# Kernel optimization log

Hardware: AMD Instinct MI355X
Metric: run time of the kernel (lower is better)

Reference implementation:

```python
import jax, jax.numpy as jnp
from jax import lax
import numpy as np

SCALE, K_UP = 2, 5


def conv2d(x, w, pad=0, dil=1):
    return lax.conv_general_dilated(x, w, (1, 1), [(pad, pad), (pad, pad)],
                                    rhs_dilation=(dil, dil),
                                    dimension_numbers=('NCHW', 'OIHW', 'NCHW'))


def cbr(x, w, g, b, pad=0, relu=True):
    # Conv (no bias) + BatchNorm (eval: running_mean=0, running_var=1, eps=1e-5) + optional ReLU
    x = conv2d(x, w, pad)
    x = x * (g / jnp.sqrt(1.0 + 1e-5))[None, :, None, None] + b[None, :, None, None]
    return jnp.maximum(x, 0.0) if relu else x


def resize_bilinear_ac(x, ho, wo):
    # bilinear interpolation, align_corners=True (matches F.interpolate)
    B, C, H, W = x.shape
    ys = jnp.linspace(0.0, H - 1.0, ho)
    xs = jnp.linspace(0.0, W - 1.0, wo)
    y0 = jnp.floor(ys).astype(jnp.int32); y1 = jnp.minimum(y0 + 1, H - 1)
    x0 = jnp.floor(xs).astype(jnp.int32); x1 = jnp.minimum(x0 + 1, W - 1)
    wy = (ys - y0).astype(x.dtype)
    wx = (xs - x0).astype(x.dtype)
    top = x[:, :, y0, :]
    bot = x[:, :, y1, :]
    v = top * (1.0 - wy)[None, None, :, None] + bot * wy[None, None, :, None]
    return v[:, :, :, x0] * (1.0 - wx) + v[:, :, :, x1] * wx


def setup_inputs() -> dict:
    key = jax.random.key(0)
    ks = jax.random.split(key, 10)
    B, CH, CL, H, W = 4, 256, 128, 64, 64
    CMID, CO, IC, KENC = 64, 128, 64, 3

    def wgt(k, shape):
        fan = int(np.prod(shape[1:]))
        return (jax.random.normal(k, shape, jnp.float32) / np.sqrt(fan)).astype(jnp.float32)

    d = {}
    d['x_h'] = jax.random.normal(ks[0], (B, CH, H, W), jnp.float32)
    d['x_l'] = jax.random.normal(ks[1], (B, CL, H * SCALE, W * SCALE), jnp.float32)
    d['w_reduce'] = wgt(ks[2], (IC, CH, 3, 3)); d['g_reduce'] = jnp.ones(IC); d['b_reduce'] = jnp.zeros(IC)
    d['w1'] = wgt(ks[3], (CMID, CH, 1, 1)); d['g1'] = jnp.ones(CMID); d['b1'] = jnp.zeros(CMID)
    d['w2'] = wgt(ks[4], (CMID, CL, 1, 1)); d['g2'] = jnp.ones(CMID); d['b2'] = jnp.zeros(CMID)
    d['w_enc'] = wgt(ks[5], (K_UP * K_UP, 2 * CMID, KENC, KENC)); d['g_enc'] = jnp.ones(K_UP * K_UP); d['b_enc'] = jnp.zeros(K_UP * K_UP)
    d['w_out1'] = wgt(ks[6], (CO, IC + CL, 3, 3)); d['g_out1'] = jnp.ones(CO); d['b_out1'] = jnp.zeros(CO)
    d['w_out2'] = wgt(ks[7], (CO, CO, 1, 1)); d['g_out2'] = jnp.ones(CO); d['b_out2'] = jnp.zeros(CO)
    return d


def reference(x_h, x_l, w_reduce, g_reduce, b_reduce, w1, g1, b1, w2, g2, b2,
              w_enc, g_enc, b_enc, w_out1, g_out1, b_out1, w_out2, g_out2, b_out2):
    b, c, h, w = x_h.shape
    h_, w_ = h * SCALE, w * SCALE
    # content encoder -> per-pixel reassembly kernels
    x1 = resize_bilinear_ac(cbr(x_h, w1, g1, b1), h_, w_)          # [b, cmid, h_, w_]
    x2 = cbr(x_l, w2, g2, b2)                                       # [b, cmid, h_, w_]
    Wm = cbr(jnp.concatenate([x1, x2], axis=1), w_enc, g_enc, b_enc, pad=1, relu=False)
    Wm = jax.nn.softmax(Wm, axis=1)                                  # [b, k_up^2, h_, w_]
    # reduced high-level features, upsampled
    xr = cbr(x_h, w_reduce, g_reduce, b_reduce, pad=1)               # [b, ic, h, w]
    xu = resize_bilinear_ac(xr, h_, w_)                              # [b, ic, h_, w_]
    # CARAFE-style reassembly: unfold(k=5, dilation=2, pad=4) expressed as
    # 25 shifted windows of the zero-padded map -> no k^2-blown buffer.
    pad = (K_UP // 2) * SCALE
    xp = jnp.pad(xu, ((0, 0), (0, 0), (pad, pad), (pad, pad)))
    X = jnp.zeros_like(xu)
    for i in range(K_UP):
        for j in range(K_UP):
            win = xp[:, :, i * SCALE:i * SCALE + h_, j * SCALE:j * SCALE + w_]
            X = X + Wm[:, i * K_UP + j][:, None] * win
    y = jnp.concatenate([X, x_l], axis=1)
    y = cbr(y, w_out1, g_out1, b_out1, pad=1)
    y = cbr(y, w_out2, g_out2, b_out2)
    return y
```

## Files before the change

kernel.cpp:

```cpp
#include <hip/hip_runtime.h>
#include <math.h>

#define BNS 0.99999500003749981f

typedef short          bf16x8  __attribute__((ext_vector_type(8)));
typedef float          f32x4   __attribute__((ext_vector_type(4)));
typedef unsigned short u16x8   __attribute__((ext_vector_type(8)));
typedef unsigned short u16x4   __attribute__((ext_vector_type(4)));
typedef unsigned short ushort_t;

__device__ inline ushort_t f2b(float f) {
    union { float f; unsigned int u; } x; x.f = f;
    unsigned int u = x.u;
    unsigned int r = (u + 0x7FFFu + ((u >> 16) & 1u)) >> 16;
    return (ushort_t)r;
}
__device__ inline float b2f(ushort_t s) {
    union { unsigned int u; float f; } x; x.u = ((unsigned int)s) << 16;
    return x.f;
}

__device__ inline void glds16(const ushort_t* gp, void* lp) {
    __builtin_amdgcn_global_load_lds(
        (const __attribute__((address_space(1))) unsigned int*)gp,
        (__attribute__((address_space(3))) unsigned int*)lp, 16, 0, 0);
}

template<int N, bool LG0>
__device__ __forceinline__ void wait_v() {
    if constexpr (LG0) {
        if constexpr (N == 0)  asm volatile("s_waitcnt vmcnt(0) lgkmcnt(0)" ::: "memory");
        if constexpr (N == 2)  asm volatile("s_waitcnt vmcnt(2) lgkmcnt(0)" ::: "memory");
        if constexpr (N == 3)  asm volatile("s_waitcnt vmcnt(3) lgkmcnt(0)" ::: "memory");
        if constexpr (N == 4)  asm volatile("s_waitcnt vmcnt(4) lgkmcnt(0)" ::: "memory");
        if constexpr (N == 5)  asm volatile("s_waitcnt vmcnt(5) lgkmcnt(0)" ::: "memory");
        if constexpr (N == 6)  asm volatile("s_waitcnt vmcnt(6) lgkmcnt(0)" ::: "memory");
        if constexpr (N == 8)  asm volatile("s_waitcnt vmcnt(8) lgkmcnt(0)" ::: "memory");
        if constexpr (N == 9)  asm volatile("s_waitcnt vmcnt(9) lgkmcnt(0)" ::: "memory");
        if constexpr (N == 10) asm volatile("s_waitcnt vmcnt(10) lgkmcnt(0)" ::: "memory");
        if constexpr (N == 12) asm volatile("s_waitcnt vmcnt(12) lgkmcnt(0)" ::: "memory");
        if constexpr (N == 16) asm volatile("s_waitcnt vmcnt(16) lgkmcnt(0)" ::: "memory");
    } else {
        if constexpr (N == 0)  asm volatile("s_waitcnt vmcnt(0)" ::: "memory");
        if constexpr (N == 2)  asm volatile("s_waitcnt vmcnt(2)" ::: "memory");
        if constexpr (N == 3)  asm volatile("s_waitcnt vmcnt(3)" ::: "memory");
        if constexpr (N == 4)  asm volatile("s_waitcnt vmcnt(4)" ::: "memory");
        if constexpr (N == 5)  asm volatile("s_waitcnt vmcnt(5)" ::: "memory");
        if constexpr (N == 6)  asm volatile("s_waitcnt vmcnt(6)" ::: "memory");
        if constexpr (N == 8)  asm volatile("s_waitcnt vmcnt(8)" ::: "memory");
        if constexpr (N == 9)  asm volatile("s_waitcnt vmcnt(9)" ::: "memory");
        if constexpr (N == 10) asm volatile("s_waitcnt vmcnt(10)" ::: "memory");
        if constexpr (N == 12) asm volatile("s_waitcnt vmcnt(12)" ::: "memory");
        if constexpr (N == 16) asm volatile("s_waitcnt vmcnt(16)" ::: "memory");
    }
}
#define WAITSW(nn, LG) do { switch (nn) {                       \
    case 0:  wait_v<0,  LG>(); break;                           \
    case 2:  wait_v<2,  LG>(); break;                           \
    case 3:  wait_v<3,  LG>(); break;                           \
    case 4:  wait_v<4,  LG>(); break;                           \
    case 5:  wait_v<5,  LG>(); break;                           \
    case 6:  wait_v<6,  LG>(); break;                           \
    case 8:  wait_v<8,  LG>(); break;                           \
    case 9:  wait_v<9,  LG>(); break;                           \
    case 10: wait_v<10, LG>(); break;                           \
    case 12: wait_v<12, LG>(); break;                           \
    default: wait_v<16, LG>(); break; } } while (0)

#define E_BWR   0u
#define E_BW1   147456u
#define E_BW2   163840u
#define E_BWE   172032u
#define E_BWO1  208896u
#define E_BWO2  430080u
#define E_ZP    446464u
#define OFF_R1  524288u
#define OFF_R4  4718592u
#define OFF_R2  8912896u
#define OFF_R3  9961472u
#define OFF_R6  11010048u
#define OFF_R5  13107200u


__device__ inline void wseg3(int idx, const float* src, ushort_t* dst,
                             int TAPS, int COT, int CIT, int CO_real) {
    int kt  = idx / (COT * 32);
    int r   = idx - kt * (COT * 32);
    int q   = r / (COT * 8);
    int r2  = r - q * (COT * 8);
    int co  = r2 >> 3;
    int e   = r2 & 7;
    int KCT = CIT >> 5;
    int tap = kt / KCT, j = kt - tap * KCT;
    int ci  = j * 32 + q * 8 + e;
    float v = (co < CO_real) ? src[((size_t)co * CIT + ci) * TAPS + tap] : 0.f;
    dst[idx] = f2b(v);
}

__device__ inline void cvt_t16(const float* __restrict__ in,
                               ushort_t* __restrict__ out,
                               int C, int LHW, int px, int npx) {
    if (px >= npx) return;
    int HW = 1 << LHW;
    int b = px >> LHW, phw = px & (HW - 1);
    const float* src = in + (size_t)b * C * HW + phw;
    unsigned base = (unsigned)(px >> 4) * (C * 16) + (unsigned)(px & 15) * 8;
    for (int c0 = 0; c0 < C; c0 += 8) {
        u16x8 o;
#pragma unroll
        for (int j = 0; j < 8; j++) o[j] = f2b(src[(size_t)(c0 + j) * HW]);
        *reinterpret_cast<u16x8*>(out + base + (c0 >> 3) * 128) = o;
    }
}

__global__ __launch_bounds__(256)
void prep_all(const float* wr, const float* w1, const float* w2,
              const float* we, const float* wo1, const float* wo2,
              const float* xh, const float* xl, ushort_t* ws0)
{
    int bx = blockIdx.x;
    int tid = threadIdx.x;
    if (bx < 1872) {
        int idx = bx * 256 + tid;
        const int n0 = 9*64*256;
        const int n1 = 64*256;
        const int n2 = 64*128;
        const int n3 = 9*32*128;
        const int n4 = 9*128*192;
        const int n5 = 128*128;
        if (idx < n0) { wseg3(idx, wr,  ws0 + E_BWR,  9, 64, 256, 64);  return; } idx -= n0;
        if (idx < n1) { wseg3(idx, w1,  ws0 + E_BW1,  1, 64, 256, 64);  return; } idx -= n1;
        if (idx < n2) { wseg3(idx, w2,  ws0 + E_BW2,  1, 64, 128, 64);  return; } idx -= n2;
        if (idx < n3) { wseg3(idx, we,  ws0 + E_BWE,  9, 32, 128, 25);  return; } idx -= n3;
        if (idx < n4) { wseg3(idx, wo1, ws0 + E_BWO1, 9, 128, 192, 128); return; } idx -= n4;
        if (idx < n5) { wseg3(idx, wo2, ws0 + E_BWO2, 1, 128, 128, 128); return; } idx -= n5;
        if (idx < 32768) ws0[E_ZP + idx] = 0;
        return;
    }
    bx -= 1872;
    if (bx < 64) { cvt_t16(xh, ws0 + OFF_R1, 256, 12, bx * 256 + tid, 16384); return; }
    bx -= 64;
    cvt_t16(xl, ws0 + OFF_R5, 128, 14, bx * 256 + tid, 65536);
}

__global__ __launch_bounds__(256)
void conv_dual(const ushort_t* __restrict__ ws0,
               unsigned offA, unsigned offWr, unsigned offW1,
               const float* __restrict__ gR, const float* __restrict__ bR,
               const float* __restrict__ g1, const float* __restrict__ b1,
               ushort_t* __restrict__ outR, ushort_t* __restrict__ outC)
{
    constexpr int BM = 64, BN = 64, KCT = 8, DEP = 3, NPH = 24;
    constexpr int MF = 2, NF = 2;
    constexpr int WOFF = BM * 64;
    constexpr int ZS   = WOFF + 4 * BN * 64;
    constexpr int BUF  = ZS + 16;
    __shared__ __align__(16) char lds[DEP * BUF];

    const unsigned nx = gridDim.x, ox = blockIdx.x;
    const unsigned qq = nx >> 3, xcd = ox & 7, k0 = ox >> 3;
    const unsigned bx = xcd * qq + k0;

    const int tid = threadIdx.x, w = tid >> 6, lane = tid & 63;
    const int l15 = lane & 15, lhi = lane >> 4;
    const int wpx = (w & 1) * 32, cw0 = (w >> 1) * 32;
    const int yb = (int)(bx & 63u);
    const unsigned pxc0 = bx * 4;

    if (tid < 4 * DEP) *(unsigned*)(lds + (tid >> 2) * BUF + ZS + (tid & 3) * 4) = 0u;

    int aA[3][MF];
#pragma unroll
    for (int dxi = 0; dxi < 3; ++dxi)
#pragma unroll
        for (int mf = 0; mf < MF; ++mf) {
            int pr = wpx + mf * 16 + l15 + dxi - 1;
            bool ok = (pr >= 0) && (pr < BM);
            aA[dxi][mf] = ok ? (((pr >> 4) << 10) + (lhi << 8) + ((pr & 15) << 4)) : ZS;
        }
    int wA[NF];
#pragma unroll
    for (int nf = 0; nf < NF; ++nf)
        wA[nf] = lhi * 1024 + (cw0 + nf * 16 + l15) * 16;

    f32x4 acc[NF][MF], acc2[NF][MF];
#pragma unroll
    for (int nf = 0; nf < NF; ++nf)
#pragma unroll
        for (int mf = 0; mf < MF; ++mf) {
            acc[nf][mf]  = (f32x4){0.f, 0.f, 0.f, 0.f};
            acc2[nf][mf] = (f32x4){0.f, 0.f, 0.f, 0.f};
        }

    auto stage = [&](int p, int bsel) {
        char* lb = lds + bsel * BUF;
        const int dyi = p >> 3, kc = p & 7;
        const int dy = dyi - 1;
        const bool rowv = (yb + dy >= 0) && (yb + dy < 64);
        unsigned s = rowv
            ? offA + (unsigned)((int)pxc0 + dy * 4 + w) * 4096u
                   + (unsigned)(kc * 512) + (unsigned)(lane * 8)
            : E_ZP + (unsigned)(lane * 8);
        glds16(ws0 + s, lb + w * 1024);
#pragma unroll
        for (int i = 0; i < 3; ++i) {
            int t3 = i * 4 + w;
            int tl = t3 >> 2, uu = t3 & 3;
            unsigned wsrc = offWr + (unsigned)(((dyi * 3 + tl) * KCT + kc) * 2048)
                          + (unsigned)(uu * 512) + (unsigned)(lane * 8);
            glds16(ws0 + wsrc, lb + WOFF + tl * 4096 + uu * 1024);
        }
        if (dyi == 1) {
            unsigned wsrc = offW1 + (unsigned)(kc * 2048)
                          + (unsigned)(w * 512) + (unsigned)(lane * 8);
            glds16(ws0 + wsrc, lb + WOFF + 3 * 4096 + w * 1024);
        }
    };

    auto step = [&](int p, int bsel) {
        const char* lb = lds + bsel * BUF;
        const int dyi = p >> 3;
        __builtin_amdgcn_s_setprio(1);
#pragma unroll
        for (int t = 0; t < 3; ++t) {
            bf16x8 af[MF], wf[NF];
#pragma unroll
            for (int mf = 0; mf < MF; ++mf)
                af[mf] = *reinterpret_cast<const bf16x8*>(lb + aA[t][mf]);
#pragma unroll
            for (int nf = 0; nf < NF; ++nf)
                wf[nf] = *reinterpret_cast<const bf16x8*>(lb + WOFF + t * 4096 + wA[nf]);
#pragma unroll
            for (int nf = 0; nf < NF; ++nf)
#pragma unroll
                for (int mf = 0; mf < MF; ++mf)
                    acc[nf][mf] = __builtin_amdgcn_mfma_f32_16x16x32_bf16(
                        wf[nf], af[mf], acc[nf][mf], 0, 0, 0);
        }
        if (dyi == 1) {
            bf16x8 af[MF], wf[NF];
#pragma unroll
            for (int mf = 0; mf < MF; ++mf)
                af[mf] = *reinterpret_cast<const bf16x8*>(lb + aA[1][mf]);
#pragma unroll
            for (int nf = 0; nf < NF; ++nf)
                wf[nf] = *reinterpret_cast<const bf16x8*>(lb + WOFF + 3 * 4096 + wA[nf]);
#pragma unroll
            for (int nf = 0; nf < NF; ++nf)
#pragma unroll
                for (int mf = 0; mf < MF; ++mf)
                    acc2[nf][mf] = __builtin_amdgcn_mfma_f32_16x16x32_bf16(
                        wf[nf], af[mf], acc2[nf][mf], 0, 0, 0);
        }
        __builtin_amdgcn_s_setprio(0);
    };

    stage(0, 0); stage(1, 1);
#pragma unroll
    for (int p = 0; p < NPH; ++p) {
        if (p + 2 < NPH) stage(p + 2, (p + 2) % 3);
        int n1 = (p + 1 < NPH) ? ((((p + 1) >> 3) == 1) ? 5 : 4) : 0;
        int n2 = (p + 2 < NPH) ? ((((p + 2) >> 3) == 1) ? 5 : 4) : 0;
        int nn = n1 + n2;
        if (p == 0) WAITSW(nn, true); else WAITSW(nn, false);
        __builtin_amdgcn_s_barrier();
        __builtin_amdgcn_sched_barrier(0);
        step(p, p % 3);
        __builtin_amdgcn_sched_barrier(0);
        if (p + 1 < NPH) __builtin_amdgcn_s_barrier();
    }

#pragma unroll
    for (int which = 0; which < 2; ++which) {
        const float* gg = which ? g1 : gR;
        const float* bb = which ? b1 : bR;
        ushort_t* oo = which ? outC : outR;
#pragma unroll
        for (int nf = 0; nf < NF; ++nf) {
            const int cg = cw0 + nf * 16 + (lhi << 2);
            float sc[4], bi[4];
#pragma unroll
            for (int r = 0; r < 4; r++) { sc[r] = gg[cg + r] * BNS; bi[r] = bb[cg + r]; }
#pragma unroll
            for (int mf = 0; mf < MF; ++mf) {
                f32x4 a = which ? acc2[nf][mf] : acc[nf][mf];
                u16x4 ov;
#pragma unroll
                for (int r = 0; r < 4; r++)
                    ov[r] = f2b(fmaxf(fmaf(a[r], sc[r], bi[r]), 0.f));
                int px = (int)bx * BM + wpx + mf * 16 + l15;
                unsigned off = (unsigned)(px >> 4) * 1024
                             + (unsigned)(cg >> 3) * 128
                             + (unsigned)(px & 15) * 8 + (unsigned)(cg & 7);
                *reinterpret_cast<u16x4*>(oo + off) = ov;
            }
        }
    }
}

template<int TAPS, int BM, int CIA, int CIB, int COT, int BN, int G,
         int WSX, int DEP, int EPI>
__global__ __launch_bounds__(256)
void conv_lds(const ushort_t* __restrict__ ws0,
              unsigned offA, unsigned offB, unsigned offW,
              const float* __restrict__ g, const float* __restrict__ bia,
              int COclamp, void* __restrict__ outp,
              int H, int LHW, int relu,
              unsigned offW2, const float* __restrict__ g2,
              const float* __restrict__ bia2)
{
    constexpr int KCA = CIA / 32, KCB = CIB / 32;
    constexpr int KCT = KCA + KCB;
    constexpr int NW  = (TAPS == 9) ? 3 : G;
    constexpr int ACP = (TAPS == 9) ? 1 : G;
    constexpr int NPH = (TAPS == 9) ? 3 * KCT : KCT / G;
    constexpr int WSY = 4 / WSX;
    constexpr int MF = BM / WSX / 16;
    constexpr int NF = BN / WSY / 16;
    constexpr int ACHUNK = BM / 16;
    constexpr int A4 = (ACP * ACHUNK + 3) / 4;
    constexpr int WUNIT = BN / 16;
    constexpr int TWU = NW * WUNIT;
    constexpr int W4 = (TWU + 3) / 4;
    constexpr int SS = A4 + W4;
    constexpr int WOFF = ACP * BM * 64;
    constexpr int ZS   = WOFF + NW * BN * 64;
    constexpr int BUF  = ZS + 16;
    constexpr int LBN3 = (BN == 128) ? 10 : (BN == 64) ? 9 : 8;
    __shared__ __align__(16) char lds[DEP * BUF];

    const unsigned nx = gridDim.x, ox = blockIdx.x;
    const unsigned qq = nx >> 3, xcd = ox & 7, k0 = ox >> 3;
    const unsigned bx = xcd * qq + k0;
    const int co_blk = blockIdx.y * BN;

    const int tid = threadIdx.x, w = tid >> 6, lane = tid & 63;
    const int l15 = lane & 15, lhi = lane >> 4;
    const int wpx = (w % WSX) * (BM / WSX);
    const int cw0 = (w / WSX) * (BN / WSY);
    const int yb = (int)(bx & (unsigned)(H - 1));
    const unsigned pxc0 = bx * ACHUNK;

    if (tid < 4 * DEP) *(unsigned*)(lds + (tid >> 2) * BUF + ZS + (tid & 3) * 4) = 0u;

    int aA[3][MF];
#pragma unroll
    for (int dxi = 0; dxi < 3; ++dxi) {
        const int dx = dxi - 1;
#pragma unroll
        for (int mf = 0; mf < MF; ++mf) {
            int pr = wpx + mf * 16 + l15 + dx;
            bool ok = (TAPS == 1) ? true : (pr >= 0 && pr < BM);
            aA[dxi][mf] = ok ? (((pr >> 4) << 10) + (lhi << 8) + ((pr & 15) << 4)) : ZS;
        }
    }
    int wA[NF];
#pragma unroll
    for (int nf = 0; nf < NF; ++nf)
        wA[nf] = (lhi * BN + cw0 + nf * 16 + l15) * 16;

    f32x4 acc[NF][MF];
#pragma unroll
    for (int nf = 0; nf < NF; ++nf)
#pragma unroll
        for (int mf = 0; mf < MF; ++mf)
            acc[nf][mf] = (f32x4){0.f, 0.f, 0.f, 0.f};

    auto stage = [&](int p, int bsel) {
        char* lb = lds + bsel * BUF;
        if constexpr (TAPS == 9) {
            const int dyi = p / KCT, kc = p - dyi * KCT;
            const int dy = dyi - 1;
            const bool isA = (kc < KCA);
            const int kcs = isA ? kc : kc - KCA;
            const int CI  = isA ? CIA : CIB;
            const unsigned offS = isA ? offA : offB;
            const bool rowv = (yb + dy >= 0) && (yb + dy < H);
#pragma unroll
            for (int i = 0; i < A4; ++i) {
                int u = (i * 4 + w) % ACHUNK;
                unsigned s = rowv
                    ? offS + (unsigned)((int)pxc0 + dy * ACHUNK + u) * (unsigned)(CI * 16)
                           + (unsigned)(kcs * 512) + (unsigned)(lane * 8)
                    : E_ZP + (unsigned)(lane * 8);
                glds16(ws0 + s, lb + u * 1024);
            }
#pragma unroll
            for (int i = 0; i < W4; ++i) {
                int t3 = (i * 4 + w) % TWU;
                int tl = t3 / WUNIT, uu = t3 - tl * WUNIT;
                unsigned wsrc = offW + (unsigned)((dyi * 3 + tl) * KCT + kc)
                                       * (unsigned)(COT * 32);
                int el  = uu * 512 + lane * 8;
                int q   = el >> LBN3;
                int col = (el & ((1 << LBN3) - 1)) >> 3;
                glds16(ws0 + wsrc + q * (COT * 8) + (co_blk + col) * 8,
                       lb + WOFF + tl * (BN * 64) + uu * 1024);
            }
        } else {
#pragma unroll
            for (int i = 0; i < A4; ++i) {
                int lin = (i * 4 + w) % (ACP * ACHUNK);
                int gc = lin / ACHUNK, u = lin - gc * ACHUNK;
                unsigned s = offA + (unsigned)(pxc0 + u) * (unsigned)(CIA * 16)
                           + (unsigned)((p * G + gc) * 512) + (unsigned)(lane * 8);
                glds16(ws0 + s, lb + gc * (BM * 64) + u * 1024);
            }
#pragma unroll
            for (int i = 0; i < W4; ++i) {
                int t3 = (i * 4 + w) % TWU;
                int tl = t3 / WUNIT, uu = t3 - tl * WUNIT;
                unsigned wsrc = offW + (unsigned)(p * G + tl) * (unsigned)(COT * 32);
                int el  = uu * 512 + lane * 8;
                int q   = el >> LBN3;
                int col = (el & ((1 << LBN3) - 1)) >> 3;
                glds16(ws0 + wsrc + q * (COT * 8) + (co_blk + col) * 8,
                       lb + WOFF + tl * (BN * 64) + uu * 1024);
            }
        }
    };

    auto step = [&](int p, int bsel) {
        const char* lb = lds + bsel * BUF;
        __builtin_amdgcn_s_setprio(1);
#pragma unroll
        for (int t = 0; t < NW; ++t) {
            const int dxi = (TAPS == 9) ? t : 1;
            const char* ab = lb + ((TAPS == 9) ? 0 : t * (BM * 64));
            bf16x8 af[MF], wf[NF];
#pragma unroll
            for (int mf = 0; mf < MF; ++mf)
                af[mf] = *reinterpret_cast<const bf16x8*>(ab + aA[dxi][mf]);
#pragma unroll
            for (int nf = 0; nf < NF; ++nf)
                wf[nf] = *reinterpret_cast<const bf16x8*>(
                    lb + WOFF + t * (BN * 64) + wA[nf]);
#pragma unroll
            for (int nf = 0; nf < NF; ++nf)
#pragma unroll
                for (int mf = 0; mf < MF; ++mf)
                    acc[nf][mf] = __builtin_amdgcn_mfma_f32_16x16x32_bf16(
                        wf[nf], af[mf], acc[nf][mf], 0, 0, 0);
        }
        __builtin_amdgcn_s_setprio(0);
    };

    stage(0, 0);
    if constexpr (DEP == 3) { if (1 < NPH) stage(1, 1); }
#pragma unroll
    for (int p = 0; p < NPH; ++p) {
        if (p + DEP - 1 < NPH) stage(p + DEP - 1, (p + DEP - 1) % DEP);
        int rem = NPH - 1 - p;
        int nn = (rem >= DEP - 1 ? DEP - 1 : rem) * SS;
        if (p == 0) WAITSW(nn, true); else WAITSW(nn, false);
        __builtin_amdgcn_s_barrier();
        __builtin_amdgcn_sched_barrier(0);
        step(p, p % DEP);
        __builtin_amdgcn_sched_barrier(0);
        if (p + 1 < NPH) __builtin_amdgcn_s_barrier();
    }

    if constexpr (EPI == 0) {
        ushort_t* o1 = (ushort_t*)outp;
#pragma unroll
        for (int nf = 0; nf < NF; ++nf) {
            const int cg = co_blk + cw0 + nf * 16 + (lhi << 2);
            float sc[4], bi[4];
#pragma unroll
            for (int r = 0; r < 4; r++) {
                int c = min(cg + r, COclamp - 1);
                sc[r] = g[c] * BNS; bi[r] = bia[c];
            }
#pragma unroll
            for (int mf = 0; mf < MF; ++mf) {
                f32x4 a = acc[nf][mf];
                u16x4 ov;
#pragma unroll
                for (int r = 0; r < 4; r++) {
                    float v = fmaf(a[r], sc[r], bi[r]);
                    if (relu) v = fmaxf(v, 0.f);
                    ov[r] = f2b(v);
                }
                int px = (int)bx * BM + wpx + mf * 16 + l15;
                unsigned off = (unsigned)(px >> 4) * (COT * 16)
                             + (unsigned)(cg >> 3) * 128
                             + (unsigned)(px & 15) * 8 + (unsigned)(cg & 7);
                *reinterpret_cast<u16x4*>(o1 + off) = ov;
            }
        }
    } else if constexpr (EPI == 1) {
        float* o1 = (float*)outp;
        const int HW = 1 << LHW;
#pragma unroll
        for (int nf = 0; nf < NF; ++nf) {
            const int cg = co_blk + cw0 + nf * 16 + (lhi << 2);
            float sc[4], bi[4];
#pragma unroll
            for (int r = 0; r < 4; r++) {
                int c = min(cg + r, COclamp - 1);
                sc[r] = g[c] * BNS; bi[r] = bia[c];
            }
#pragma unroll
            for (int mf = 0; mf < MF; ++mf) {
                int px = (int)bx * BM + wpx + mf * 16 + l15;
                int b = px >> LHW, phw = px & (HW - 1);
#pragma unroll
                for (int r = 0; r < 4; r++) {
                    float v = fmaf(acc[nf][mf][r], sc[r], bi[r]);
                    if (relu) v = fmaxf(v, 0.f);
                    o1[((size_t)(b * COT + cg + r)) * HW + phw] = v;
                }
            }
        }
    } else if constexpr (EPI == 2) {
        __syncthreads();
        float* sf = (float*)lds;
#pragma unroll
        for (int nf = 0; nf < NF; ++nf) {
            const int cg = cw0 + nf * 16 + (lhi << 2);
#pragma unroll
            for (int mf = 0; mf < MF; ++mf) {
                int pxl = wpx + mf * 16 + l15;
                f32x4 a = acc[nf][mf];
#pragma unroll
                for (int r = 0; r < 4; r++) {
                    int c = min(cg + r, COclamp - 1);
                    sf[(cg + r) * 136 + pxl] = fmaf(a[r], g[c] * BNS, bia[c]);
                }
            }
        }
        __syncthreads();
        if (tid < BM) {
            int gpx = (int)bx * BM + tid;
            float v[25];
#pragma unroll
            for (int c = 0; c < 25; ++c) v[c] = sf[c * 136 + tid];
            float m = v[0];
#pragma unroll
            for (int c = 1; c < 25; ++c) m = fmaxf(m, v[c]);
            float s = 0.f;
#pragma unroll
            for (int c = 0; c < 25; ++c) { v[c] = __expf(v[c] - m); s += v[c]; }
            float inv = 1.f / s;
            ushort_t* o1 = (ushort_t*)outp;
            unsigned base = (unsigned)(gpx >> 4) * (32 * 16) + (unsigned)(gpx & 15) * 8;
#pragma unroll
            for (int q = 0; q < 3; ++q) {
                u16x8 ov;
#pragma unroll
                for (int k = 0; k < 8; k++) ov[k] = f2b(v[q * 8 + k] * inv);
                *reinterpret_cast<u16x8*>(o1 + base + q * 128) = ov;
            }
            o1[base + 384] = f2b(v[24] * inv);
        }
    } else {
#pragma unroll
        for (int nf = 0; nf < NF; ++nf) {
            const int cg = cw0 + nf * 16 + (lhi << 2);
            float sc[4], bi[4];
#pragma unroll
            for (int r = 0; r < 4; r++) { sc[r] = g[cg + r] * BNS; bi[r] = bia[cg + r]; }
#pragma unroll
            for (int mf = 0; mf < MF; ++mf) {
                f32x4 a = acc[nf][mf];
                u16x4 ov;
#pragma unroll
                for (int r = 0; r < 4; r++)
                    ov[r] = f2b(fmaxf(fmaf(a[r], sc[r], bi[r]), 0.f));
                int pxl = wpx + mf * 16 + l15;
                unsigned off = (unsigned)(pxl >> 4) * 4096
                             + (unsigned)(cg >> 5) * 1024
                             + (unsigned)((cg >> 3) & 3) * 256
                             + (unsigned)(pxl & 15) * 16 + (unsigned)(cg & 7) * 2;
                *reinterpret_cast<u16x4*>((char*)lds + off) = ov;
            }
        }
        __syncthreads();
#pragma unroll
        for (int i = 0; i < 8; ++i) {
            int U = i * 4 + w;
            glds16(ws0 + offW2 + (unsigned)U * 512 + (unsigned)(lane * 8),
                   lds + BUF + U * 1024);
        }
        wait_v<0, true>();
        __builtin_amdgcn_s_barrier();
        __builtin_amdgcn_sched_barrier(0);
        f32x4 acc2[NF][MF];
#pragma unroll
        for (int nf = 0; nf < NF; ++nf)
#pragma unroll
            for (int mf = 0; mf < MF; ++mf)
                acc2[nf][mf] = (f32x4){0.f, 0.f, 0.f, 0.f};
        __builtin_amdgcn_s_setprio(1);
#pragma unroll
        for (int kc = 0; kc < 4; ++kc) {
            bf16x8 af[MF], wf[NF];
#pragma unroll
            for (int mf = 0; mf < MF; ++mf) {
                int pxl = wpx + mf * 16 + l15;
                af[mf] = *reinterpret_cast<const bf16x8*>(
                    (char*)lds + (pxl >> 4) * 4096 + kc * 1024
                               + (lhi << 8) + (pxl & 15) * 16);
            }
#pragma unroll
            for (int nf = 0; nf < NF; ++nf)
                wf[nf] = *reinterpret_cast<const bf16x8*>(
                    (char*)lds + BUF + kc * 8192 + wA[nf]);
#pragma unroll
            for (int nf = 0; nf < NF; ++nf)
#pragma unroll
                for (int mf = 0; mf < MF; ++mf)
                    acc2[nf][mf] = __builtin_amdgcn_mfma_f32_16x16x32_bf16(
                        wf[nf], af[mf], acc2[nf][mf], 0, 0, 0);
        }
        __builtin_amdgcn_s_setprio(0);
        __syncthreads();
        float* o1 = (float*)outp;
        float* sf = (float*)lds;
        const int phw_base = (int)((bx & 127u) * 128);
        const int bimg = (int)(bx >> 7);
        const int lane32 = tid & 31, cog = tid >> 5;
#pragma unroll
        for (int c = 0; c < 2; ++c) {
            if (c) __syncthreads();
            if (cw0 == c * 64) {
#pragma unroll
                for (int nf = 0; nf < NF; ++nf) {
                    const int cgl = nf * 16 + (lhi << 2);
                    const int cg  = c * 64 + cgl;
                    float sc[4], bi[4];
#pragma unroll
                    for (int r = 0; r < 4; r++) { sc[r] = g2[cg + r] * BNS; bi[r] = bia2[cg + r]; }
#pragma unroll
                    for (int mf = 0; mf < MF; ++mf) {
                        int pxl = wpx + mf * 16 + l15;
                        f32x4 a = acc2[nf][mf];
#pragma unroll
                        for (int r = 0; r < 4; r++)
                            sf[(cgl + r) * 132 + pxl] =
                                fmaxf(fmaf(a[r], sc[r], bi[r]), 0.f);
                    }
                }
            }
            __syncthreads();
#pragma unroll
            for (int j = 0; j < 8; ++j) {
                int col = cog + j * 8;
                f32x4 v = *reinterpret_cast<const f32x4*>(sf + col * 132 + lane32 * 4);
                *reinterpret_cast<f32x4*>(
                    o1 + (((size_t)bimg * 128 + c * 64 + col) << 14)
                       + phw_base + lane32 * 4) = v;
            }
        }
    }
}

__global__ __launch_bounds__(256)
void resize2x_t16(const ushort_t* __restrict__ in, ushort_t* __restrict__ out)
{
    int t = blockIdx.x * 256 + threadIdx.x;
    int cg = t & 7;
    int opx = t >> 3;
    int xo = opx & 127;
    int rest = opx >> 7;
    int yo = rest & 127;
    int b  = rest >> 7;
    float fy = (float)yo * 63.f / 127.f;
    float fx = (float)xo * 63.f / 127.f;
    int y0 = (int)fy, x0 = (int)fx;
    float wy = fy - (float)y0, wx = fx - (float)x0;
    int y1 = min(y0 + 1, 63), x1 = min(x0 + 1, 63);
    int qb = b * 4096;
#define RD(Y, X) (*reinterpret_cast<const bf16x8*>(in + \
    (unsigned)(((qb + (Y) * 64 + (X)) >> 4) * 1024) + cg * 128 + ((qb + (Y) * 64 + (X)) & 15) * 8))
    bf16x8 v00 = RD(y0, x0), v01 = RD(y0, x1), v10 = RD(y1, x0), v11 = RD(y1, x1);
#undef RD
    u16x8 o;
#pragma unroll
    for (int k = 0; k < 8; k++) {
        float l = b2f((ushort_t)v00[k]) * (1.f - wy) + b2f((ushort_t)v10[k]) * wy;
        float r = b2f((ushort_t)v01[k]) * (1.f - wy) + b2f((ushort_t)v11[k]) * wy;
        o[k] = f2b(l * (1.f - wx) + r * wx);
    }
    *reinterpret_cast<u16x8*>(out + (unsigned)(opx >> 4) * 1024 + cg * 128 + (opx & 15) * 8) = o;
}

__global__ __launch_bounds__(256)
void carafe25(const ushort_t* __restrict__ wm, const ushort_t* __restrict__ xu,
              ushort_t* __restrict__ out)
{
    int t = blockIdx.x * 256 + threadIdx.x;
    int cg = t & 7;
    int px = t >> 3;
    int x = px & 127;
    int y = (px >> 7) & 127;
    const ushort_t* wp = wm + (unsigned)(px >> 4) * 512 + (px & 15) * 8;
    u16x8 r0 = *reinterpret_cast<const u16x8*>(wp);
    u16x8 r1 = *reinterpret_cast<const u16x8*>(wp + 128);
    u16x8 r2 = *reinterpret_cast<const u16x8*>(wp + 256);
    float v[25];
#pragma unroll
    for (int k = 0; k < 8; k++) v[k]      = b2f(r0[k]);
#pragma unroll
    for (int k = 0; k < 8; k++) v[8 + k]  = b2f(r1[k]);
#pragma unroll
    for (int k = 0; k < 8; k++) v[16 + k] = b2f(r2[k]);
    v[24] = b2f(wp[384]);

    float acc[8];
#pragma unroll
    for (int k = 0; k < 8; k++) acc[k] = 0.f;
#pragma unroll
    for (int i = 0; i < 5; i++) {
        int yy = y + 2 * i - 4;
#pragma unroll
        for (int j = 0; j < 5; j++) {
            int xx = x + 2 * j - 4;
            if (yy >= 0 && yy < 128 && xx >= 0 && xx < 128) {
                int q = px + (2 * i - 4) * 128 + (2 * j - 4);
                bf16x8 xv = *reinterpret_cast<const bf16x8*>(
                    xu + (unsigned)(q >> 4) * 1024 + cg * 128 + (q & 15) * 8);
                float wv = v[i * 5 + j];
#pragma unroll
                for (int k = 0; k < 8; k++)
                    acc[k] = fmaf(wv, b2f((ushort_t)xv[k]), acc[k]);
            }
        }
    }
    u16x8 o;
#pragma unroll
    for (int k = 0; k < 8; k++) o[k] = f2b(acc[k]);
    *reinterpret_cast<u16x8*>(out + (unsigned)(px >> 4) * 1024 + cg * 128 + (px & 15) * 8) = o;
}

extern "C" void kernel_launch(void* const* d_in, const int* in_sizes, int n_in,
                              void* d_out, int out_size, void* d_ws, size_t ws_size,
                              hipStream_t stream)
{
    const float* x_h      = (const float*)d_in[0];
    const float* x_l      = (const float*)d_in[1];
    const float* w_reduce = (const float*)d_in[2];
    const float* g_reduce = (const float*)d_in[3];
    const float* b_reduce = (const float*)d_in[4];
    const float* w1       = (const float*)d_in[5];
    const float* g1       = (const float*)d_in[6];
    const float* b1       = (const float*)d_in[7];
    const float* w2       = (const float*)d_in[8];
    const float* g2       = (const float*)d_in[9];
    const float* b2       = (const float*)d_in[10];
    const float* w_enc    = (const float*)d_in[11];
    const float* g_enc    = (const float*)d_in[12];
    const float* b_enc    = (const float*)d_in[13];
    const float* w_out1   = (const float*)d_in[14];
    const float* g_out1   = (const float*)d_in[15];
    const float* b_out1   = (const float*)d_in[16];
    const float* w_out2   = (const float*)d_in[17];
    const float* g_out2   = (const float*)d_in[18];
    const float* b_out2   = (const float*)d_in[19];

    ushort_t* ws0 = (ushort_t*)d_ws;

    const unsigned oXHC = OFF_R1;
    const unsigned oC1  = OFF_R2;
    const unsigned oXR  = OFF_R3;
    const unsigned oX1  = OFF_R4;
    const unsigned oXLC = OFF_R5;
    const unsigned oX2  = OFF_R1;
    const unsigned oWM  = OFF_R6;
    const unsigned oXU  = OFF_R4;
    const unsigned oXB  = OFF_R1;

    prep_all<<<2192, 256, 0, stream>>>(w_reduce, w1, w2, w_enc, w_out1, w_out2,
                                       x_h, x_l, ws0);
    conv_dual<<<256, 256, 0, stream>>>(
        ws0, oXHC, E_BWR, E_BW1, g_reduce, b_reduce, g1, b1,
        ws0 + oXR, ws0 + oC1);
    resize2x_t16<<<2048, 256, 0, stream>>>(ws0 + oC1, ws0 + oX1);
    conv_lds<1, 128, 128, 0, 64, 64, 1, 2, 3, 0><<<dim3(512, 1), 256, 0, stream>>>(
        ws0, oXLC, 0u, E_BW2, g2, b2, 64, ws0 + oX2, 128, 14, 1,
        0u, nullptr, nullptr);
    conv_lds<9, 128, 64, 64, 32, 32, 1, 4, 3, 2><<<dim3(512, 1), 256, 0, stream>>>(
        ws0, oX1, oX2, E_BWE, g_enc, b_enc, 25, ws0 + oWM, 128, 14, 0,
        0u, nullptr, nullptr);
    resize2x_t16<<<2048, 256, 0, stream>>>(ws0 + oXR, ws0 + oXU);
    carafe25<<<2048, 256, 0, stream>>>(ws0 + oWM, ws0 + oXU, ws0 + oXB);
    conv_lds<9, 128, 64, 128, 128, 128, 1, 2, 2, 4><<<dim3(512, 1), 256, 0, stream>>>(
        ws0, oXB, oXLC, E_BWO1, g_out1, b_out1, 128, d_out, 128, 14, 1,
        E_BWO2, g_out2, b_out2);
}
```

Measured before the change: 128.7 us.

## Split conv_dual output channels across two blocks to double grid size

The fused reduce/1x1 conv kernel now launches a 2D grid, with each block computing 32 of the 64 output channels instead of all 64, which doubles the number of blocks from 256 to 512. Weight staging is rewritten to load only the block's channel half, using a modular unit index for the extra 1x1 weights in the middle row phase, and per-wave accumulators shrink to one N fragment. The intent is to fill more CUs on the GPU. The cost is that each activation tile is now loaded twice, once per channel half, and each wave issues fewer MFMAs per LDS read.

```diff
diff --git a/kernel.cpp b/kernel.cpp
--- a/kernel.cpp
+++ b/kernel.cpp
@@ -150,20 +150,20 @@
                const float* __restrict__ g1, const float* __restrict__ b1,
                ushort_t* __restrict__ outR, ushort_t* __restrict__ outC)
 {
-    constexpr int BM = 64, BN = 64, KCT = 8, DEP = 3, NPH = 24;
-    constexpr int MF = 2, NF = 2;
-    constexpr int WOFF = BM * 64;
-    constexpr int ZS   = WOFF + 4 * BN * 64;
+    constexpr int DEP = 3, NPH = 24, KCT = 8;
+    constexpr int MF = 2;
+    constexpr int WOFF = 4096;
+    constexpr int ZS   = WOFF + 4 * 2048;
     constexpr int BUF  = ZS + 16;
     __shared__ __align__(16) char lds[DEP * BUF];
 
-    const unsigned nx = gridDim.x, ox = blockIdx.x;
-    const unsigned qq = nx >> 3, xcd = ox & 7, k0 = ox >> 3;
-    const unsigned bx = xcd * qq + k0;
+    const unsigned ox = blockIdx.x;
+    const unsigned bx = (ox & 7) * 32 + (ox >> 3);
+    const int co_blk = blockIdx.y * 32;
 
     const int tid = threadIdx.x, w = tid >> 6, lane = tid & 63;
     const int l15 = lane & 15, lhi = lane >> 4;
-    const int wpx = (w & 1) * 32, cw0 = (w >> 1) * 32;
+    const int wpx = (w & 1) * 32, cw0 = (w >> 1) * 16;
     const int yb = (int)(bx & 63u);
     const unsigned pxc0 = bx * 4;
 
@@ -175,22 +175,17 @@
 #pragma unroll
         for (int mf = 0; mf < MF; ++mf) {
             int pr = wpx + mf * 16 + l15 + dxi - 1;
-            bool ok = (pr >= 0) && (pr < BM);
+            bool ok = (pr >= 0) && (pr < 64);
             aA[dxi][mf] = ok ? (((pr >> 4) << 10) + (lhi << 8) + ((pr & 15) << 4)) : ZS;
         }
-    int wA[NF];
-#pragma unroll
-    for (int nf = 0; nf < NF; ++nf)
-        wA[nf] = lhi * 1024 + (cw0 + nf * 16 + l15) * 16;
-
-    f32x4 acc[NF][MF], acc2[NF][MF];
-#pragma unroll
-    for (int nf = 0; nf < NF; ++nf)
-#pragma unroll
-        for (int mf = 0; mf < MF; ++mf) {
-            acc[nf][mf]  = (f32x4){0.f, 0.f, 0.f, 0.f};
-            acc2[nf][mf] = (f32x4){0.f, 0.f, 0.f, 0.f};
-        }
+    const int wA = (lhi * 32 + cw0 + l15) * 16;
+
+    f32x4 acc[MF], acc2[MF];
+#pragma unroll
+    for (int mf = 0; mf < MF; ++mf) {
+        acc[mf]  = (f32x4){0.f, 0.f, 0.f, 0.f};
+        acc2[mf] = (f32x4){0.f, 0.f, 0.f, 0.f};
+    }
 
     auto stage = [&](int p, int bsel) {
         char* lb = lds + bsel * BUF;
@@ -202,18 +197,20 @@
                    + (unsigned)(kc * 512) + (unsigned)(lane * 8)
             : E_ZP + (unsigned)(lane * 8);
         glds16(ws0 + s, lb + w * 1024);
-#pragma unroll
-        for (int i = 0; i < 3; ++i) {
-            int t3 = i * 4 + w;
-            int tl = t3 >> 2, uu = t3 & 3;
-            unsigned wsrc = offWr + (unsigned)(((dyi * 3 + tl) * KCT + kc) * 2048)
-                          + (unsigned)(uu * 512) + (unsigned)(lane * 8);
-            glds16(ws0 + wsrc, lb + WOFF + tl * 4096 + uu * 1024);
-        }
-        if (dyi == 1) {
-            unsigned wsrc = offW1 + (unsigned)(kc * 2048)
-                          + (unsigned)(w * 512) + (unsigned)(lane * 8);
-            glds16(ws0 + wsrc, lb + WOFF + 3 * 4096 + w * 1024);
+        const int nunits = (dyi == 1) ? 8 : 6;
+#pragma unroll
+        for (int i = 0; i < 2; ++i) {
+            int t3 = (i * 4 + w) % nunits;
+            int tl = t3 >> 1, uu = t3 & 1;
+            int el  = uu * 512 + lane * 8;
+            int q   = el >> 8;
+            int col = (el & 255) >> 3;
+            unsigned src = (tl < 3)
+                ? offWr + (unsigned)(((dyi * 3 + tl) * KCT + kc) * 2048)
+                        + (unsigned)(q * 512) + (unsigned)((co_blk + col) * 8)
+                : offW1 + (unsigned)(kc * 2048)
+                        + (unsigned)(q * 512) + (unsigned)((co_blk + col) * 8);
+            glds16(ws0 + src, lb + WOFF + tl * 2048 + uu * 1024);
         }
     };
 
@@ -223,34 +220,26 @@
         __builtin_amdgcn_s_setprio(1);
 #pragma unroll
         for (int t = 0; t < 3; ++t) {
-            bf16x8 af[MF], wf[NF];
+            bf16x8 af[MF];
 #pragma unroll
             for (int mf = 0; mf < MF; ++mf)
                 af[mf] = *reinterpret_cast<const bf16x8*>(lb + aA[t][mf]);
-#pragma unroll
-            for (int nf = 0; nf < NF; ++nf)
-                wf[nf] = *reinterpret_cast<const bf16x8*>(lb + WOFF + t * 4096 + wA[nf]);
-#pragma unroll
-            for (int nf = 0; nf < NF; ++nf)
-#pragma unroll
-                for (int mf = 0; mf < MF; ++mf)
-                    acc[nf][mf] = __builtin_amdgcn_mfma_f32_16x16x32_bf16(
-                        wf[nf], af[mf], acc[nf][mf], 0, 0, 0);
+            bf16x8 wf = *reinterpret_cast<const bf16x8*>(lb + WOFF + t * 2048 + wA);
+#pragma unroll
+            for (int mf = 0; mf < MF; ++mf)
+                acc[mf] = __builtin_amdgcn_mfma_f32_16x16x32_bf16(
+                    wf, af[mf], acc[mf], 0, 0, 0);
         }
         if (dyi == 1) {
-            bf16x8 af[MF], wf[NF];
+            bf16x8 af[MF];
 #pragma unroll
             for (int mf = 0; mf < MF; ++mf)
                 af[mf] = *reinterpret_cast<const bf16x8*>(lb + aA[1][mf]);
-#pragma unroll
-            for (int nf = 0; nf < NF; ++nf)
-                wf[nf] = *reinterpret_cast<const bf16x8*>(lb + WOFF + 3 * 4096 + wA[nf]);
-#pragma unroll
-            for (int nf = 0; nf < NF; ++nf)
-#pragma unroll
-                for (int mf = 0; mf < MF; ++mf)
-                    acc2[nf][mf] = __builtin_amdgcn_mfma_f32_16x16x32_bf16(
-                        wf[nf], af[mf], acc2[nf][mf], 0, 0, 0);
+            bf16x8 wf = *reinterpret_cast<const bf16x8*>(lb + WOFF + 3 * 2048 + wA);
+#pragma unroll
+            for (int mf = 0; mf < MF; ++mf)
+                acc2[mf] = __builtin_amdgcn_mfma_f32_16x16x32_bf16(
+                    wf, af[mf], acc2[mf], 0, 0, 0);
         }
         __builtin_amdgcn_s_setprio(0);
     };
@@ -259,9 +248,8 @@
 #pragma unroll
     for (int p = 0; p < NPH; ++p) {
         if (p + 2 < NPH) stage(p + 2, (p + 2) % 3);
-        int n1 = (p + 1 < NPH) ? ((((p + 1) >> 3) == 1) ? 5 : 4) : 0;
-        int n2 = (p + 2 < NPH) ? ((((p + 2) >> 3) == 1) ? 5 : 4) : 0;
-        int nn = n1 + n2;
+        int rem = NPH - 1 - p;
+        int nn = (rem >= 2 ? 2 : rem) * 3;
         if (p == 0) WAITSW(nn, true); else WAITSW(nn, false);
         __builtin_amdgcn_s_barrier();
         __builtin_amdgcn_sched_barrier(0);
@@ -275,25 +263,22 @@
         const float* gg = which ? g1 : gR;
         const float* bb = which ? b1 : bR;
         ushort_t* oo = which ? outC : outR;
-#pragma unroll
-        for (int nf = 0; nf < NF; ++nf) {
-            const int cg = cw0 + nf * 16 + (lhi << 2);
-            float sc[4], bi[4];
-#pragma unroll
-            for (int r = 0; r < 4; r++) { sc[r] = gg[cg + r] * BNS; bi[r] = bb[cg + r]; }
-#pragma unroll
-            for (int mf = 0; mf < MF; ++mf) {
-                f32x4 a = which ? acc2[nf][mf] : acc[nf][mf];
-                u16x4 ov;
-#pragma unroll
-                for (int r = 0; r < 4; r++)
-                    ov[r] = f2b(fmaxf(fmaf(a[r], sc[r], bi[r]), 0.f));
-                int px = (int)bx * BM + wpx + mf * 16 + l15;
-                unsigned off = (unsigned)(px >> 4) * 1024
-                             + (unsigned)(cg >> 3) * 128
-                             + (unsigned)(px & 15) * 8 + (unsigned)(cg & 7);
-                *reinterpret_cast<u16x4*>(oo + off) = ov;
-            }
+        const int cg = co_blk + cw0 + (lhi << 2);
+        float sc[4], bi[4];
+#pragma unroll
+        for (int r = 0; r < 4; r++) { sc[r] = gg[cg + r] * BNS; bi[r] = bb[cg + r]; }
+#pragma unroll
+        for (int mf = 0; mf < MF; ++mf) {
+            f32x4 a = which ? acc2[mf] : acc[mf];
+            u16x4 ov;
+#pragma unroll
+            for (int r = 0; r < 4; r++)
+                ov[r] = f2b(fmaxf(fmaf(a[r], sc[r], bi[r]), 0.f));
+            int px = (int)bx * 64 + wpx + mf * 16 + l15;
+            unsigned off = (unsigned)(px >> 4) * 1024
+                         + (unsigned)(cg >> 3) * 128
+                         + (unsigned)(px & 15) * 8 + (unsigned)(cg & 7);
+            *reinterpret_cast<u16x4*>(oo + off) = ov;
         }
     }
 }
@@ -772,7 +757,7 @@
 
     prep_all<<<2192, 256, 0, stream>>>(w_reduce, w1, w2, w_enc, w_out1, w_out2,
                                        x_h, x_l, ws0);
-    conv_dual<<<256, 256, 0, stream>>>(
+    conv_dual<<<dim3(256, 2), 256, 0, stream>>>(
         ws0, oXHC, E_BWR, E_BW1, g_reduce, b_reduce, g1, b1,
         ws0 + oXR, ws0 + oC1);
     resize2x_t16<<<2048, 256, 0, stream>>>(ws0 + oC1, ws0 + oX1);
```

Result: no change. 129.4 us (+0.5%).
